# Kernel tuning notes

Hardware: AMD Instinct MI355X
Metric: run time of the kernel (lower is better)

The kernel has to match this reference:

```python
import jax, jax.numpy as jnp
import numpy as np

N, H, E, K = 256, 128, 64, 4  # nodes, hidden, dist-embed dim, heads
ALPHA = 0.2  # leaky-relu slope


def setup_inputs() -> dict:
    key = jax.random.key(0)
    ks = jax.random.split(key, 12)
    s = lambda k, sh: (jax.random.normal(k, sh, jnp.float32) * 0.05)
    return dict(
        action_hidden_state=jax.random.normal(ks[0], (N, H), jnp.float32),
        goal_hidden_state=jax.random.normal(ks[1], (N, H), jnp.float32),
        goal=jax.random.normal(ks[2], (N, 2), jnp.float32),
        action=jax.random.normal(ks[3], (N, 2), jnp.float32),
        W_emb=s(ks[4], (1, E)), b_emb=jnp.zeros((E,), jnp.float32),
        W_gate=s(ks[5], (2 * E + 2 * H, H)), b_gate=jnp.zeros((H,), jnp.float32),
        W_gat=s(ks[6], (K, H, H)), a_src=s(ks[7], (K, H)), a_dst=s(ks[8], (K, H)),
        gat_bias=jnp.zeros((H,), jnp.float32),
    )


def cal_dist(goal, action):
    # Vectorized, math-faithful (incl. source typos) version of the O(n^2) loop.
    ax, ay = action[:, 0], action[:, 1]
    gx, gy = goal[:, 0], goal[:, 1]
    a1x, a1y = ax[:, None], ay[:, None]   # node i
    a2x, a2y = ax[None, :], ay[None, :]   # node j
    g1x, g1y = gx[:, None], gy[:, None]
    g2x, g2y = gx[None, :], gy[None, :]
    dn = (a1x - a1x) * (g1y - g2y) - (a1y - a2y) * (g1x - g2x)
    cross_a = a1x * a2y - a1y * a2x
    gterm = g1x * g2y - g1x * g2x
    n1 = cross_a * (g1x - g2x) - (a1x - a2x) * gterm
    n2 = cross_a * (g1y - g2y) - (a1y - a2x) * gterm
    safe = jnp.where(dn == 0.0, 1.0, dn)
    p1, p2 = n1 / safe, n2 / safe
    base = jnp.linalg.norm(action - goal, axis=-1)  # [n]
    d1p = jnp.sqrt((a1x - p1) ** 2 + (a1y - p2) ** 2)
    d2p = jnp.sqrt((a2x - p1) ** 2 + (a2y - p2) ** 2)
    cond = (dn != 0.0) & ((a1x - p1) * (p1 - g1x) > 0.0)
    ones = jnp.ones_like(dn)
    d1 = jnp.where(cond, d1p, base[:, None] * ones)
    d2 = jnp.where(cond, d2p, base[None, :] * ones)
    n = d1.shape[0]
    ii = jnp.arange(n)[:, None]
    jj = jnp.arange(n)[None, :]
    # dist[i,j]=d1(i,j) for i<j; dist[j,i]=d2(i,j) i.e. lower triangle = d2.T; diag = |a_i - g_i|
    return jnp.where(ii == jj, base[:, None] * ones, jnp.where(ii < jj, d1, d2.T))


def reference(action_hidden_state, goal_hidden_state, goal, action,
              W_emb, b_emb, W_gate, b_gate, W_gat, a_src, a_dst, gat_bias):
    ha, hg = action_hidden_state, goal_hidden_state
    n, h = ha.shape
    dist = cal_dist(goal, action)                      # [n,n]
    emb = dist[..., None] * W_emb[0] + b_emb           # Linear(1,E) -> [n,n,E]
    # pairwise interaction gate (i != idx branch, computed for all pairs)
    gate_in = jnp.concatenate([
        jnp.broadcast_to(ha[:, None, :], (n, n, h)),
        jnp.broadcast_to(ha[None, :, :], (n, n, h)),
        emb, jnp.swapaxes(emb, 0, 1)], axis=-1)        # [n,n,2H+2E]
    gate = jax.nn.sigmoid(gate_in @ W_gate + b_gate)   # [n,n,H]
    gated = ha[None, :, :] * gate
    # self branch: gates the goal hidden state; action row stays ungated
    emb_d = emb[jnp.arange(n), jnp.arange(n)]          # [n,E]
    gate_self = jax.nn.sigmoid(
        jnp.concatenate([ha, hg, emb_d, emb_d], axis=-1) @ W_gate + b_gate)
    curr_goal = hg * gate_self                         # [n,H]
    eye = jnp.eye(n, dtype=bool)[..., None]
    curr_action = jnp.where(eye, ha[:, None, :], gated)          # [n,n,H]
    gat_in = jnp.concatenate([curr_action, curr_goal[:, None, :]], axis=1)  # [n,n+1,H]
    # multi-head GAT layer (batched over the n query nodes)
    hp = jnp.einsum('bmf,kfo->bkmo', gat_in, W_gat)    # [n,K,m,H]
    attn = (jnp.einsum('bkmo,ko->bkm', hp, a_src)[..., :, None]
            + jnp.einsum('bkmo,ko->bkm', hp, a_dst)[..., None, :])  # [n,K,m,m]
    attn = jax.nn.softmax(jax.nn.leaky_relu(attn, ALPHA), axis=-1)
    out = jnp.einsum('bkij,bkjo->bkio', attn, hp).mean(axis=1) + gat_bias  # [n,m,H]
    out = jax.nn.elu(out)
    idx = jnp.arange(n)
    return out[idx, idx]                               # [n,H]
```

## Files before the change

### kernel.cpp

```cpp
#include <hip/hip_runtime.h>
#include <math.h>

#define N 256
#define H 128
#define E 64
#define K 4
#define M (N + 1)
#define WAVES 16
#define BLOCK 1024

__device__ __forceinline__ float sigm(float x) {
    return __fdividef(1.0f, 1.0f + __expf(-x));
}

__device__ __forceinline__ float wave_sum(float v) {
#pragma unroll
    for (int d = 1; d < 64; d <<= 1) v += __shfl_xor(v, d, 64);
    return v;
}

__device__ __forceinline__ float kbutterfly(float q0, float q1, float q2, float q3,
                                            int lane) {
    const bool b1 = lane & 1;
    const bool b2 = lane & 2;
    float aA = b1 ? q1 : q0, aB = b1 ? q0 : q1;
    aA += __shfl_xor(aB, 1, 64);
    float cA = b1 ? q3 : q2, cB = b1 ? q2 : q3;
    cA += __shfl_xor(cB, 1, 64);
    float eA = b2 ? cA : aA, eB = b2 ? aA : cA;
    eA += __shfl_xor(eB, 2, 64);
#pragma unroll
    for (int d = 4; d < 64; d <<= 1) eA += __shfl_xor(eA, d, 64);
    return eA;
}

__device__ __forceinline__ void pairdist(
    float a1x, float a1y, float a2x, float a2y,
    float g1x, float g1y, float g2x, float g2y,
    float baseR, float baseC, float& d_rc, float& d_cr)
{
    float t  = __fmul_rn(__fsub_rn(a1y, a2y), __fsub_rn(g1x, g2x));
    float dn = -t;
    float ca = __fsub_rn(__fmul_rn(a1x, a2y), __fmul_rn(a1y, a2x));
    float gt = __fsub_rn(__fmul_rn(g1x, g2y), __fmul_rn(g1x, g2x));
    float n1 = __fsub_rn(__fmul_rn(ca, __fsub_rn(g1x, g2x)),
                         __fmul_rn(__fsub_rn(a1x, a2x), gt));
    float n2 = __fsub_rn(__fmul_rn(ca, __fsub_rn(g1y, g2y)),
                         __fmul_rn(__fsub_rn(a1y, a2x), gt));
    float safe = (dn == 0.0f) ? 1.0f : dn;
    float p1 = __fdiv_rn(n1, safe);
    float p2 = __fdiv_rn(n2, safe);
    bool cond = (dn != 0.0f) &&
                (__fmul_rn(__fsub_rn(a1x, p1), __fsub_rn(p1, g1x)) > 0.0f);
    float dx1 = __fsub_rn(a1x, p1), dy1 = __fsub_rn(a1y, p2);
    float d1p = __fsqrt_rn(__fadd_rn(__fmul_rn(dx1, dx1), __fmul_rn(dy1, dy1)));
    float dx2 = __fsub_rn(a2x, p1), dy2 = __fsub_rn(a2y, p2);
    float d2p = __fsqrt_rn(__fadd_rn(__fmul_rn(dx2, dx2), __fmul_rn(dy2, dy2)));
    d_rc = cond ? d1p : baseR;
    d_cr = cond ? d2p : baseC;
}

__global__ __launch_bounds__(BLOCK) void gat_pre(
    const float* __restrict__ ha, const float* __restrict__ hg,
    const float* __restrict__ W_emb, const float* __restrict__ b_emb,
    const float* __restrict__ W_gate, const float* __restrict__ b_gate,
    const float* __restrict__ W_gat, const float* __restrict__ a_src,
    const float* __restrict__ a_dst,
    float* __restrict__ A1, float* __restrict__ A2, float* __restrict__ G2,
    float* __restrict__ u3g, float* __restrict__ u4g, float* __restrict__ ccg,
    float* __restrict__ vsrc, float* __restrict__ vdst)
{
    const int b    = blockIdx.x;
    const int tid  = threadIdx.x;
    const int wid  = tid >> 6;
    const int lane = tid & 63;

    __shared__ float sRed[8][3][H];

    {
        const int f  = tid & (H - 1);
        const int sl = tid >> 7;
        const int g0 = sl * 16;
        float s1 = 0.f, s2 = 0.f, s3 = 0.f;
#pragma unroll
        for (int g = 0; g < 16; ++g) {
            const int gg = g0 + g;
            float w1 = W_gate[gg * H + f];
            float w2 = W_gate[(H + gg) * H + f];
            float av = ha[b * H + gg];
            float gv = hg[b * H + gg];
            s1 += av * w1;
            s2 += av * w2;
            s3 += gv * w2;
        }
        sRed[sl][0][f] = s1;
        sRed[sl][1][f] = s2;
        sRed[sl][2][f] = s3;
    }
    __syncthreads();
    if (tid < H) {
        float r1 = 0.f, r2 = 0.f, r3 = 0.f;
#pragma unroll
        for (int sl = 0; sl < 8; ++sl) {
            r1 += sRed[sl][0][tid];
            r2 += sRed[sl][1][tid];
            r3 += sRed[sl][2][tid];
        }
        A1[b * H + tid] = r1;
        A2[b * H + tid] = r2;
        G2[b * H + tid] = r3;
    }

    if (b < 8) {
        const int k = b >> 1;
        const float2 as = *(const float2*)&a_src[k * H + lane * 2];
        const float2 ad = *(const float2*)&a_dst[k * H + lane * 2];
#pragma unroll
        for (int it = 0; it < 4; ++it) {
            const int pair = b * 64 + wid * 4 + it;
            const int f    = pair & (H - 1);
            const float2 w = *(const float2*)&W_gat[(k * H + f) * H + lane * 2];
            float vs = wave_sum(w.x * as.x + w.y * as.y);
            float vv = wave_sum(w.x * ad.x + w.y * ad.y);
            if (lane == 0) { vsrc[k * H + f] = vs; vdst[k * H + f] = vv; }
        }
    } else if (b == 8) {
        __syncthreads();
        const int f  = tid & (H - 1);
        const int sl = tid >> 7;
        float s3 = 0.f, s4 = 0.f, scc = 0.f;
#pragma unroll
        for (int e0 = 0; e0 < 8; ++e0) {
            const int e = sl * 8 + e0;
            float w3 = W_gate[(2 * H + e) * H + f];
            float w4 = W_gate[(2 * H + E + e) * H + f];
            float we = W_emb[e], be = b_emb[e];
            s3  += we * w3;
            s4  += we * w4;
            scc += be * (w3 + w4);
        }
        sRed[sl][0][f] = s3;
        sRed[sl][1][f] = s4;
        sRed[sl][2][f] = scc;
        __syncthreads();
        if (tid < H) {
            float r3 = 0.f, r4 = 0.f, rc = 0.f;
#pragma unroll
            for (int sl = 0; sl < 8; ++sl) {
                r3 += sRed[sl][0][tid];
                r4 += sRed[sl][1][tid];
                rc += sRed[sl][2][tid];
            }
            u3g[tid] = r3;
            u4g[tid] = r4;
            ccg[tid] = rc + b_gate[tid];
        }
    }
}

__global__ __launch_bounds__(BLOCK) void gat_main(
    const float* __restrict__ ha, const float* __restrict__ hg,
    const float* __restrict__ W_gat, const float* __restrict__ gat_bias,
    const float* __restrict__ A1, const float* __restrict__ A2,
    const float* __restrict__ G2,
    const float* __restrict__ u3a, const float* __restrict__ u4a,
    const float* __restrict__ cca,
    const float* __restrict__ vsrc, const float* __restrict__ vdst,
    const float* __restrict__ goal, const float* __restrict__ action,
    float* __restrict__ out)
{
    const int i    = blockIdx.x;
    const int tid  = threadIdx.x;
    const int wid  = tid >> 6;
    const int lane = tid & 63;
    const int f0   = lane * 2;

    __shared__ float2 sAct[N];
    __shared__ float2 sGoal[N];
    __shared__ float  sBase[N];
    __shared__ float2 sD[M];
    __shared__ __align__(16) float pbuf[M * K + 4];
    __shared__ float  ssc[K];
    __shared__ float  sMred[WAVES];
    __shared__ float  sLpart[WAVES];
    __shared__ float  sLk[K];
    __shared__ float  sWfin[K][H];
    __shared__ __align__(16) char uBuf[34048];
    float* uPart = (float*)uBuf;
    float (*uSW)[K][H]  = (float (*)[K][H])uBuf;
    float (*uEp)[H]     = (float (*)[H])uBuf;

    const float2 a1v = *(const float2*)&A1[i * H + f0];
    const float2 haI = *(const float2*)&ha[i * H + f0];
    const float2 hgI = *(const float2*)&hg[i * H + f0];
    const float2 g2v = *(const float2*)&G2[i * H + f0];
    const float2 u3  = *(const float2*)&u3a[f0];
    const float2 u4  = *(const float2*)&u4a[f0];
    const float2 cc  = *(const float2*)&cca[f0];
    const float2 vd0 = *(const float2*)&vdst[0 * H + f0];
    const float2 vd1 = *(const float2*)&vdst[1 * H + f0];
    const float2 vd2 = *(const float2*)&vdst[2 * H + f0];
    const float2 vd3 = *(const float2*)&vdst[3 * H + f0];
    const float2 vs0 = *(const float2*)&vsrc[0 * H + f0];
    const float2 vs1 = *(const float2*)&vsrc[1 * H + f0];
    const float2 vs2 = *(const float2*)&vsrc[2 * H + f0];
    const float2 vs3 = *(const float2*)&vsrc[3 * H + f0];

    for (int t = tid; t < N; t += BLOCK) {
        float2 a = ((const float2*)action)[t];
        float2 g = ((const float2*)goal)[t];
        sAct[t]  = a;
        sGoal[t] = g;
        float dx = __fsub_rn(a.x, g.x), dy = __fsub_rn(a.y, g.y);
        sBase[t] = __fsqrt_rn(__fadd_rn(__fmul_rn(dx, dx), __fmul_rn(dy, dy)));
    }
    __syncthreads();

    if (tid < M) {
        const int j = tid;
        float dij = 0.f, dji = 0.f;
        if (j != i && j != N) {
            const float2 aI = sAct[i], gI = sGoal[i];
            const float2 aJ = sAct[j], gJ = sGoal[j];
            if (i < j)
                pairdist(aI.x, aI.y, aJ.x, aJ.y, gI.x, gI.y, gJ.x, gJ.y,
                         sBase[i], sBase[j], dij, dji);
            else
                pairdist(aJ.x, aJ.y, aI.x, aI.y, gJ.x, gJ.y, gI.x, gI.y,
                         sBase[j], sBase[i], dji, dij);
        }
        sD[j] = make_float2(dij, dji);
    }

    const float scOwn = kbutterfly(haI.x * vs0.x + haI.y * vs0.y,
                                   haI.x * vs1.x + haI.y * vs1.y,
                                   haI.x * vs2.x + haI.y * vs2.y,
                                   haI.x * vs3.x + haI.y * vs3.y, lane);
    if (wid == 0 && lane < K) ssc[lane] = scOwn;

    const float2 a1cc = make_float2(a1v.x + cc.x, a1v.y + cc.y);
    const float baseI = sBase[i];
    __syncthreads();

    const bool b1 = lane & 1;
    const bool b2 = lane & 2;
    const int  wrIdx   = ((lane >> 3) << 2) + (lane & 3);
    const bool doWrite = !(lane & 4);
    float2 gin[16];

#pragma unroll
    for (int t = 0; t < 16; ++t) {
        const int jj = wid + 16 * t;
        const float2 a2 = *(const float2*)&A2[jj * H + f0];
        const float2 hj = *(const float2*)&ha[jj * H + f0];
        const float2 d  = sD[jj];
        float tx = a1cc.x + a2.x + d.x * u3.x + d.y * u4.x;
        float ty = a1cc.y + a2.y + d.x * u3.y + d.y * u4.y;
        float2 g = make_float2(hj.x * sigm(tx), hj.y * sigm(ty));
        if (jj == i) g = haI;
        gin[t] = g;
        float q0 = g.x * vd0.x + g.y * vd0.y;
        float q1 = g.x * vd1.x + g.y * vd1.y;
        float q2 = g.x * vd2.x + g.y * vd2.y;
        float q3 = g.x * vd3.x + g.y * vd3.y;
        float aA = b1 ? q1 : q0, aB = b1 ? q0 : q1;
        aA += __shfl_xor(aB, 1, 64);
        float cA = b1 ? q3 : q2, cB = b1 ? q2 : q3;
        cA += __shfl_xor(cB, 1, 64);
        float eA = b2 ? cA : aA, eB = b2 ? aA : cA;
        eA += __shfl_xor(eB, 2, 64);
        eA += __shfl_xor(eA, 4, 64);
        if (doWrite) uPart[jj * 33 + wrIdx] = eA;
    }

    float2 ginG = make_float2(0.f, 0.f);
    if (wid == 0) {
        float tx = a1cc.x + g2v.x + baseI * (u3.x + u4.x);
        float ty = a1cc.y + g2v.y + baseI * (u3.y + u4.y);
        ginG = make_float2(hgI.x * sigm(tx), hgI.y * sigm(ty));
        float q0 = ginG.x * vd0.x + ginG.y * vd0.y;
        float q1 = ginG.x * vd1.x + ginG.y * vd1.y;
        float q2 = ginG.x * vd2.x + ginG.y * vd2.y;
        float q3 = ginG.x * vd3.x + ginG.y * vd3.y;
        float aA = b1 ? q1 : q0, aB = b1 ? q0 : q1;
        aA += __shfl_xor(aB, 1, 64);
        float cA = b1 ? q3 : q2, cB = b1 ? q2 : q3;
        cA += __shfl_xor(cB, 1, 64);
        float eA = b2 ? cA : aA, eB = b2 ? aA : cA;
        eA += __shfl_xor(eB, 2, 64);
        eA += __shfl_xor(eA, 4, 64);
        if (doWrite) uPart[N * 33 + wrIdx] = eA;
    }
    __syncthreads();

    const int jq = tid & 255;
    const int kq = tid >> 8;
    float dd = 0.f;
#pragma unroll
    for (int g = 0; g < 8; ++g) dd += uPart[jq * 33 + g * 4 + kq];
    float lgq = ssc[kq] + dd;
    lgq = (lgq >= 0.f) ? lgq : 0.2f * lgq;

    float lgT = -INFINITY;
    if (tid < 4) {
        float ddT = 0.f;
#pragma unroll
        for (int g = 0; g < 8; ++g) ddT += uPart[N * 33 + g * 4 + tid];
        lgT = ssc[tid] + ddT;
        lgT = (lgT >= 0.f) ? lgT : 0.2f * lgT;
    }

    float mx = fmaxf(lgq, lgT);
#pragma unroll
    for (int d = 1; d < 64; d <<= 1) mx = fmaxf(mx, __shfl_xor(mx, d, 64));
    if (lane == 0) sMred[wid] = mx;
    __syncthreads();

    float Mg = sMred[0];
#pragma unroll
    for (int w = 1; w < WAVES; ++w) Mg = fmaxf(Mg, sMred[w]);

    const float pq = __expf(lgq - Mg);
    pbuf[jq * 4 + kq] = pq;
    if (tid < 4) pbuf[N * 4 + tid] = __expf(lgT - Mg);

    const float lp = wave_sum(pq);
    if (lane == 0) sLpart[wid] = lp;
    __syncthreads();
    if (tid < 4)
        sLk[tid] = sLpart[tid * 4 + 0] + sLpart[tid * 4 + 1] +
                   sLpart[tid * 4 + 2] + sLpart[tid * 4 + 3] +
                   pbuf[N * 4 + tid];

    float w00 = 0.f, w01 = 0.f, w02 = 0.f, w03 = 0.f;
    float w10 = 0.f, w11 = 0.f, w12 = 0.f, w13 = 0.f;
#pragma unroll
    for (int t = 0; t < 16; ++t) {
        const int jj = wid + 16 * t;
        const float4 p4 = *(const float4*)&pbuf[jj * 4];
        w00 += p4.x * gin[t].x;  w10 += p4.x * gin[t].y;
        w01 += p4.y * gin[t].x;  w11 += p4.y * gin[t].y;
        w02 += p4.z * gin[t].x;  w12 += p4.z * gin[t].y;
        w03 += p4.w * gin[t].x;  w13 += p4.w * gin[t].y;
    }
    if (wid == 0) {
        const float4 p4 = *(const float4*)&pbuf[N * 4];
        w00 += p4.x * ginG.x;  w10 += p4.x * ginG.y;
        w01 += p4.y * ginG.x;  w11 += p4.y * ginG.y;
        w02 += p4.z * ginG.x;  w12 += p4.z * ginG.y;
        w03 += p4.w * ginG.x;  w13 += p4.w * ginG.y;
    }

    *(float2*)&uSW[wid][0][f0] = make_float2(w00, w10);
    *(float2*)&uSW[wid][1][f0] = make_float2(w01, w11);
    *(float2*)&uSW[wid][2][f0] = make_float2(w02, w12);
    *(float2*)&uSW[wid][3][f0] = make_float2(w03, w13);
    __syncthreads();

    if (tid < K * H) {
        const int k = tid >> 7;
        const int f = tid & (H - 1);
        float W = 0.f;
#pragma unroll
        for (int w = 0; w < WAVES; ++w) W += uSW[w][k][f];
        sWfin[k][f] = W / sLk[k];
    }
    __syncthreads();

    {
        const int f = tid & (H - 1);
        const int s = tid >> 7;
        float acc = 0.0f;
#pragma unroll
        for (int k = 0; k < K; ++k) {
            const int g0 = s * 16;
#pragma unroll
            for (int g = 0; g < 16; ++g)
                acc += sWfin[k][g0 + g] * W_gat[(k * H + g0 + g) * H + f];
        }
        __syncthreads();
        uEp[s][f] = acc;
    }
    __syncthreads();

    if (tid < H) {
        float acc = 0.0f;
#pragma unroll
        for (int s = 0; s < 8; ++s) acc += uEp[s][tid];
        float val = 0.25f * acc + gat_bias[tid];
        out[i * H + tid] = (val > 0.0f) ? val : expm1f(val);
    }
}

extern "C" void kernel_launch(void* const* d_in, const int* in_sizes, int n_in,
                              void* d_out, int out_size, void* d_ws, size_t ws_size,
                              hipStream_t stream)
{
    const float* ha       = (const float*)d_in[0];
    const float* hg       = (const float*)d_in[1];
    const float* goal     = (const float*)d_in[2];
    const float* action   = (const float*)d_in[3];
    const float* W_emb    = (const float*)d_in[4];
    const float* b_emb    = (const float*)d_in[5];
    const float* W_gate   = (const float*)d_in[6];
    const float* b_gate   = (const float*)d_in[7];
    const float* W_gat    = (const float*)d_in[8];
    const float* a_src    = (const float*)d_in[9];
    const float* a_dst    = (const float*)d_in[10];
    const float* gat_bias = (const float*)d_in[11];

    float* ws  = (float*)d_ws;
    float* A1  = ws;
    float* A2  = A1 + N * H;
    float* G2  = A2 + N * H;
    float* u3  = G2 + N * H;
    float* u4  = u3 + H;
    float* cc  = u4 + H;
    float* vs  = cc + H;
    float* vd  = vs + K * H;

    hipLaunchKernelGGL(gat_pre, dim3(N), dim3(BLOCK), 0, stream,
                       ha, hg, W_emb, b_emb, W_gate, b_gate,
                       W_gat, a_src, a_dst,
                       A1, A2, G2, u3, u4, cc, vs, vd);

    hipLaunchKernelGGL(gat_main, dim3(N), dim3(BLOCK), 0, stream,
                       ha, hg, W_gat, gat_bias,
                       A1, A2, G2, u3, u4, cc, vs, vd,
                       goal, action, (float*)d_out);
}
```

Measured before the change: 28.05 us.

## Fuse GAT softmax into the gated-feature loop and drop max-shift barriers

Attention logits, exponentials, the softmax denominator and the weighted feature sums are now computed inside the per-neighbour loop. Each wave does a full in-register butterfly reduce and broadcasts the per-head probabilities with readlane. This removes the shared logit buffer, the block-wide max reduction, the probability buffer and several __syncthreads. The gin register array is no longer kept live. In exchange the max-subtraction stability step is dropped, so large logits could overflow in __expf. Each neighbour also now needs more shuffles than the earlier partial reduce.

```diff
diff --git a/kernel.cpp b/kernel.cpp
--- a/kernel.cpp
+++ b/kernel.cpp
@@ -17,6 +17,10 @@
 #pragma unroll
     for (int d = 1; d < 64; d <<= 1) v += __shfl_xor(v, d, 64);
     return v;
+}
+
+__device__ __forceinline__ float readlane_f(float v, int l) {
+    return __uint_as_float(__builtin_amdgcn_readlane(__float_as_uint(v), l));
 }
 
 __device__ __forceinline__ float kbutterfly(float q0, float q1, float q2, float q3,
@@ -179,16 +183,10 @@
     __shared__ float2 sGoal[N];
     __shared__ float  sBase[N];
     __shared__ float2 sD[M];
-    __shared__ __align__(16) float pbuf[M * K + 4];
-    __shared__ float  ssc[K];
-    __shared__ float  sMred[WAVES];
-    __shared__ float  sLpart[WAVES];
-    __shared__ float  sLk[K];
+    __shared__ float  sW[WAVES][K][H];
+    __shared__ float  sL[WAVES][K];
     __shared__ float  sWfin[K][H];
-    __shared__ __align__(16) char uBuf[34048];
-    float* uPart = (float*)uBuf;
-    float (*uSW)[K][H]  = (float (*)[K][H])uBuf;
-    float (*uEp)[H]     = (float (*)[H])uBuf;
+    __shared__ float  sPart[8][H];
 
     const float2 a1v = *(const float2*)&A1[i * H + f0];
     const float2 haI = *(const float2*)&ha[i * H + f0];
@@ -236,17 +234,14 @@
                                    haI.x * vs1.x + haI.y * vs1.y,
                                    haI.x * vs2.x + haI.y * vs2.y,
                                    haI.x * vs3.x + haI.y * vs3.y, lane);
-    if (wid == 0 && lane < K) ssc[lane] = scOwn;
 
     const float2 a1cc = make_float2(a1v.x + cc.x, a1v.y + cc.y);
     const float baseI = sBase[i];
     __syncthreads();
 
-    const bool b1 = lane & 1;
-    const bool b2 = lane & 2;
-    const int  wrIdx   = ((lane >> 3) << 2) + (lane & 3);
-    const bool doWrite = !(lane & 4);
-    float2 gin[16];
+    float l_ = 0.f;
+    float w00 = 0.f, w01 = 0.f, w02 = 0.f, w03 = 0.f;
+    float w10 = 0.f, w11 = 0.f, w12 = 0.f, w13 = 0.f;
 
 #pragma unroll
     for (int t = 0; t < 16; ++t) {
@@ -258,103 +253,55 @@
         float ty = a1cc.y + a2.y + d.x * u3.y + d.y * u4.y;
         float2 g = make_float2(hj.x * sigm(tx), hj.y * sigm(ty));
         if (jj == i) g = haI;
-        gin[t] = g;
+
         float q0 = g.x * vd0.x + g.y * vd0.y;
         float q1 = g.x * vd1.x + g.y * vd1.y;
         float q2 = g.x * vd2.x + g.y * vd2.y;
         float q3 = g.x * vd3.x + g.y * vd3.y;
-        float aA = b1 ? q1 : q0, aB = b1 ? q0 : q1;
-        aA += __shfl_xor(aB, 1, 64);
-        float cA = b1 ? q3 : q2, cB = b1 ? q2 : q3;
-        cA += __shfl_xor(cB, 1, 64);
-        float eA = b2 ? cA : aA, eB = b2 ? aA : cA;
-        eA += __shfl_xor(eB, 2, 64);
-        eA += __shfl_xor(eA, 4, 64);
-        if (doWrite) uPart[jj * 33 + wrIdx] = eA;
-    }
-
-    float2 ginG = make_float2(0.f, 0.f);
+        float e  = kbutterfly(q0, q1, q2, q3, lane);
+
+        float lg = scOwn + e;
+        lg = (lg >= 0.f) ? lg : 0.2f * lg;
+        const float p = __expf(lg);
+        l_ += p;
+
+        const float p0 = readlane_f(p, 0), p1 = readlane_f(p, 1);
+        const float p2 = readlane_f(p, 2), p3 = readlane_f(p, 3);
+        w00 += p0 * g.x;  w10 += p0 * g.y;
+        w01 += p1 * g.x;  w11 += p1 * g.y;
+        w02 += p2 * g.x;  w12 += p2 * g.y;
+        w03 += p3 * g.x;  w13 += p3 * g.y;
+    }
+
     if (wid == 0) {
         float tx = a1cc.x + g2v.x + baseI * (u3.x + u4.x);
         float ty = a1cc.y + g2v.y + baseI * (u3.y + u4.y);
-        ginG = make_float2(hgI.x * sigm(tx), hgI.y * sigm(ty));
-        float q0 = ginG.x * vd0.x + ginG.y * vd0.y;
-        float q1 = ginG.x * vd1.x + ginG.y * vd1.y;
-        float q2 = ginG.x * vd2.x + ginG.y * vd2.y;
-        float q3 = ginG.x * vd3.x + ginG.y * vd3.y;
-        float aA = b1 ? q1 : q0, aB = b1 ? q0 : q1;
-        aA += __shfl_xor(aB, 1, 64);
-        float cA = b1 ? q3 : q2, cB = b1 ? q2 : q3;
-        cA += __shfl_xor(cB, 1, 64);
-        float eA = b2 ? cA : aA, eB = b2 ? aA : cA;
-        eA += __shfl_xor(eB, 2, 64);
-        eA += __shfl_xor(eA, 4, 64);
-        if (doWrite) uPart[N * 33 + wrIdx] = eA;
-    }
-    __syncthreads();
-
-    const int jq = tid & 255;
-    const int kq = tid >> 8;
-    float dd = 0.f;
-#pragma unroll
-    for (int g = 0; g < 8; ++g) dd += uPart[jq * 33 + g * 4 + kq];
-    float lgq = ssc[kq] + dd;
-    lgq = (lgq >= 0.f) ? lgq : 0.2f * lgq;
-
-    float lgT = -INFINITY;
-    if (tid < 4) {
-        float ddT = 0.f;
-#pragma unroll
-        for (int g = 0; g < 8; ++g) ddT += uPart[N * 33 + g * 4 + tid];
-        lgT = ssc[tid] + ddT;
-        lgT = (lgT >= 0.f) ? lgT : 0.2f * lgT;
-    }
-
-    float mx = fmaxf(lgq, lgT);
-#pragma unroll
-    for (int d = 1; d < 64; d <<= 1) mx = fmaxf(mx, __shfl_xor(mx, d, 64));
-    if (lane == 0) sMred[wid] = mx;
-    __syncthreads();
-
-    float Mg = sMred[0];
-#pragma unroll
-    for (int w = 1; w < WAVES; ++w) Mg = fmaxf(Mg, sMred[w]);
-
-    const float pq = __expf(lgq - Mg);
-    pbuf[jq * 4 + kq] = pq;
-    if (tid < 4) pbuf[N * 4 + tid] = __expf(lgT - Mg);
-
-    const float lp = wave_sum(pq);
-    if (lane == 0) sLpart[wid] = lp;
-    __syncthreads();
-    if (tid < 4)
-        sLk[tid] = sLpart[tid * 4 + 0] + sLpart[tid * 4 + 1] +
-                   sLpart[tid * 4 + 2] + sLpart[tid * 4 + 3] +
-                   pbuf[N * 4 + tid];
-
-    float w00 = 0.f, w01 = 0.f, w02 = 0.f, w03 = 0.f;
-    float w10 = 0.f, w11 = 0.f, w12 = 0.f, w13 = 0.f;
-#pragma unroll
-    for (int t = 0; t < 16; ++t) {
-        const int jj = wid + 16 * t;
-        const float4 p4 = *(const float4*)&pbuf[jj * 4];
-        w00 += p4.x * gin[t].x;  w10 += p4.x * gin[t].y;
-        w01 += p4.y * gin[t].x;  w11 += p4.y * gin[t].y;
-        w02 += p4.z * gin[t].x;  w12 += p4.z * gin[t].y;
-        w03 += p4.w * gin[t].x;  w13 += p4.w * gin[t].y;
-    }
-    if (wid == 0) {
-        const float4 p4 = *(const float4*)&pbuf[N * 4];
-        w00 += p4.x * ginG.x;  w10 += p4.x * ginG.y;
-        w01 += p4.y * ginG.x;  w11 += p4.y * ginG.y;
-        w02 += p4.z * ginG.x;  w12 += p4.z * ginG.y;
-        w03 += p4.w * ginG.x;  w13 += p4.w * ginG.y;
-    }
-
-    *(float2*)&uSW[wid][0][f0] = make_float2(w00, w10);
-    *(float2*)&uSW[wid][1][f0] = make_float2(w01, w11);
-    *(float2*)&uSW[wid][2][f0] = make_float2(w02, w12);
-    *(float2*)&uSW[wid][3][f0] = make_float2(w03, w13);
+        float2 g = make_float2(hgI.x * sigm(tx), hgI.y * sigm(ty));
+
+        float q0 = g.x * vd0.x + g.y * vd0.y;
+        float q1 = g.x * vd1.x + g.y * vd1.y;
+        float q2 = g.x * vd2.x + g.y * vd2.y;
+        float q3 = g.x * vd3.x + g.y * vd3.y;
+        float e  = kbutterfly(q0, q1, q2, q3, lane);
+
+        float lg = scOwn + e;
+        lg = (lg >= 0.f) ? lg : 0.2f * lg;
+        const float p = __expf(lg);
+        l_ += p;
+
+        const float p0 = readlane_f(p, 0), p1 = readlane_f(p, 1);
+        const float p2 = readlane_f(p, 2), p3 = readlane_f(p, 3);
+        w00 += p0 * g.x;  w10 += p0 * g.y;
+        w01 += p1 * g.x;  w11 += p1 * g.y;
+        w02 += p2 * g.x;  w12 += p2 * g.y;
+        w03 += p3 * g.x;  w13 += p3 * g.y;
+    }
+
+    *(float2*)&sW[wid][0][f0] = make_float2(w00, w10);
+    *(float2*)&sW[wid][1][f0] = make_float2(w01, w11);
+    *(float2*)&sW[wid][2][f0] = make_float2(w02, w12);
+    *(float2*)&sW[wid][3][f0] = make_float2(w03, w13);
+    if (lane < K) sL[wid][lane] = l_;
     __syncthreads();
 
     if (tid < K * H) {
@@ -362,8 +309,11 @@
         const int f = tid & (H - 1);
         float W = 0.f;
 #pragma unroll
-        for (int w = 0; w < WAVES; ++w) W += uSW[w][k][f];
-        sWfin[k][f] = W / sLk[k];
+        for (int w = 0; w < WAVES; ++w) W += sW[w][k][f];
+        float L = 0.f;
+#pragma unroll
+        for (int w = 0; w < WAVES; ++w) L += sL[w][k];
+        sWfin[k][f] = W / L;
     }
     __syncthreads();
 
@@ -378,15 +328,14 @@
             for (int g = 0; g < 16; ++g)
                 acc += sWfin[k][g0 + g] * W_gat[(k * H + g0 + g) * H + f];
         }
-        __syncthreads();
-        uEp[s][f] = acc;
+        sPart[s][f] = acc;
     }
     __syncthreads();
 
     if (tid < H) {
         float acc = 0.0f;
 #pragma unroll
-        for (int s = 0; s < 8; ++s) acc += uEp[s][tid];
+        for (int s = 0; s < 8; ++s) acc += sPart[s][tid];
         float val = 0.25f * acc + gat_bias[tid];
         out[i * H + tid] = (val > 0.0f) ? val : expm1f(val);
     }
```

Result: no change. 28.47 us (+1.5%).
